# Optimization experiments

Measured on AMD Instinct MI355X. Metric: run time of the kernel, lower is better.

Reference implementation:

```python
import jax, jax.numpy as jnp
import numpy as np

N_NODES = 100000
N_EDGES = 1600000
B = 16
NMAX = 4096
IN_DIM = 32
H1 = 64      # capacity C
H2 = 128     # 2C
LAT = 64
DEC_H = 128  # 2C
DEC_IN = LAT + 2
FUEL = 5


def _ln(x, g, b):
    m = x.mean(-1, keepdims=True)
    v = x.var(-1, keepdims=True)
    return (x - m) / jnp.sqrt(v + 1e-5) * g + b


def _mlp2(x, wi, bi, g, be, wo, bo):
    # DeepMLP with num_layers=2: in_lin -> LayerNorm -> ReLU -> out_lin
    h = jax.nn.relu(_ln(x @ wi + bi, g, be))
    return h @ wo + bo


def setup_inputs() -> dict:
    key = jax.random.key(0)
    ks = jax.random.split(key, 48)
    d = {}
    d['x'] = jax.random.normal(ks[0], (N_NODES, IN_DIM), jnp.float32)
    d['edge_index'] = jax.random.randint(ks[1], (2, N_EDGES), 0, N_NODES)
    d['batch'] = jnp.sort(jax.random.randint(ks[2], (N_NODES,), 0, B))

    def w(k, shape):
        return (jax.random.normal(k, shape, jnp.float32) * 0.02)

    conv_shapes = {'w1m': (IN_DIM, H1), 'w2m': (H1, H2), 'w3m': (H2, LAT),
                   'w1l': (IN_DIM, H1), 'w2l': (H1, H2), 'w3l': (H2, LAT)}
    i = 3
    for nm, sh in conv_shapes.items():
        d[nm] = w(ks[i], sh); i += 1
        d['b' + nm[1:]] = jnp.zeros((sh[1],), jnp.float32)
    # node_mlp (DeepMLP dec_in->dec_h->dec_h)
    d['nm_wi'] = w(ks[i], (DEC_IN, DEC_H)); i += 1
    d['nm_bi'] = jnp.zeros((DEC_H,), jnp.float32)
    d['nm_g'] = jnp.ones((DEC_H,), jnp.float32)
    d['nm_be'] = jnp.zeros((DEC_H,), jnp.float32)
    d['nm_wo'] = w(ks[i], (DEC_H, DEC_H)); i += 1
    d['nm_bo'] = jnp.zeros((DEC_H,), jnp.float32)
    # heads
    d['ex_w'] = w(ks[i], (DEC_H, 1)); i += 1
    d['ex_b'] = jnp.zeros((1,), jnp.float32)
    d['fu_w'] = w(ks[i], (DEC_H, FUEL)); i += 1
    d['fu_b'] = jnp.zeros((FUEL,), jnp.float32)
    d['al_w'] = w(ks[i], (DEC_H, 1)); i += 1
    d['al_b'] = jnp.zeros((1,), jnp.float32)
    d['sl_w'] = w(ks[i], (DEC_H, 1)); i += 1
    d['sl_b'] = jnp.zeros((1,), jnp.float32)
    # edge_mlp (DeepMLP dec_in->dec_h->8)
    d['em_wi'] = w(ks[i], (DEC_IN, DEC_H)); i += 1
    d['em_bi'] = jnp.zeros((DEC_H,), jnp.float32)
    d['em_g'] = jnp.ones((DEC_H,), jnp.float32)
    d['em_be'] = jnp.zeros((DEC_H,), jnp.float32)
    d['em_wo'] = w(ks[i], (DEC_H, 8)); i += 1
    d['em_bo'] = jnp.zeros((8,), jnp.float32)
    d['pos_all'] = jax.random.normal(ks[i], (NMAX, 2), jnp.float32)
    return d


def reference(x, edge_index, batch,
              w1m, b1m, w2m, b2m, w3m, b3m,
              w1l, b1l, w2l, b2l, w3l, b3l,
              nm_wi, nm_bi, nm_g, nm_be, nm_wo, nm_bo,
              ex_w, ex_b, fu_w, fu_b, al_w, al_b, sl_w, sl_b,
              em_wi, em_bi, em_g, em_be, em_wo, em_bo,
              pos_all):
    # ---- GCN encoder with self-loops and symmetric normalization (PyG GCNConv) ----
    loops = jnp.arange(N_NODES)
    src = jnp.concatenate([edge_index[0], loops])
    dst = jnp.concatenate([edge_index[1], loops])
    deg = jax.ops.segment_sum(jnp.ones(src.shape, jnp.float32), dst, N_NODES)
    dinv = jax.lax.rsqrt(deg)  # deg >= 1 because of self-loops
    norm = (dinv[src] * dinv[dst])[:, None]

    def conv(h, wt, bt):
        hw = h @ wt                                   # [N, F_out]
        return jax.ops.segment_sum(norm * hw[src], dst, N_NODES) + bt

    mu = jax.nn.relu(conv(x, w1m, b1m))
    mu = jax.nn.relu(conv(mu, w2m, b2m))
    mu = jax.nn.relu(conv(mu, w3m, b3m))
    lg = jax.nn.relu(conv(x, w1l, b1l))
    lg = jax.nn.relu(conv(lg, w2l, b2l))
    lg = jax.nn.relu(conv(lg, w3l, b3l))

    cnt = jnp.maximum(jax.ops.segment_sum(jnp.ones((N_NODES,), jnp.float32), batch, B), 1.0)[:, None]
    mu_g = jax.ops.segment_sum(mu, batch, B) / cnt    # global_mean_pool [B, LAT]
    lg_g = jax.ops.segment_sum(lg, batch, B) / cnt

    z = mu_g  # eval-mode latent_sample returns mu

    # ---- decoder ----
    Z = jnp.broadcast_to(z[:, None, :], (B, NMAX, LAT))
    pos = jnp.broadcast_to(pos_all[None], (B, NMAX, 2))
    Zp = jnp.concatenate([Z, pos], -1).reshape(B * NMAX, DEC_IN)
    h = _mlp2(Zp, nm_wi, nm_bi, nm_g, nm_be, nm_wo, nm_bo)
    nodes = (h @ ex_w + ex_b).reshape(B, NMAX, 1)
    fuel = (h @ fu_w + fu_b).reshape(B, NMAX, FUEL)
    alt = (h @ al_w + al_b).reshape(B, NMAX, 1)
    slope = (h @ sl_w + sl_b).reshape(B, NMAX, 1)
    edges = _mlp2(Zp, em_wi, em_bi, em_g, em_be, em_wo, em_bo).reshape(B, NMAX, 8)
    return (nodes, edges, fuel, alt, slope, mu_g, lg_g)
```

## Files before the change

### kernel.cpp

```cpp
#include <hip/hip_runtime.h>
#include <hip/hip_bf16.h>

#define N_NODES 100000
#define N_EDGESC 1600000
#define BATCH_B 16
#define NMAXC 4096
#define LATC 64
#define NBINS 391
#define NSB 256
#define EPB ((N_EDGESC + NSB - 1) / NSB)
#define BIN_PAD 768

#define OUT_NODES 0
#define OUT_EDGES 65536
#define OUT_FUEL  589824
#define OUT_ALT   917504
#define OUT_SLOPE 983040
#define OUT_MU    1048576
#define OUT_LG    1049600

typedef float f32x2 __attribute__((ext_vector_type(2)));
typedef float f32x4 __attribute__((ext_vector_type(4)));
typedef short bf16x8 __attribute__((ext_vector_type(8)));
union U4B { uint4 u; bf16x8 b; };

__device__ __forceinline__ unsigned short f2bf(float f) {
    unsigned int u = __float_as_uint(f);
    return (unsigned short)((u + 0x7FFFu + ((u >> 16) & 1u)) >> 16);
}
__device__ __forceinline__ float bf2f(unsigned short h) {
    return __uint_as_float(((unsigned int)h) << 16);
}
__device__ __forceinline__ void f8acc(unsigned int u, float& a0, float& a1, float& a2, float& a3) {
    f32x2 lo = __builtin_amdgcn_cvt_pk_f32_fp8(u, false);
    f32x2 hi = __builtin_amdgcn_cvt_pk_f32_fp8(u, true);
    a0 += lo[0]; a1 += lo[1]; a2 += hi[0]; a3 += hi[1];
}
__device__ __forceinline__ void f8_to_bf2(unsigned int u, unsigned int& q0, unsigned int& q1) {
    f32x2 lo = __builtin_amdgcn_cvt_pk_f32_fp8(u, false);
    f32x2 hi = __builtin_amdgcn_cvt_pk_f32_fp8(u, true);
    q0 = (unsigned int)f2bf(lo[0]) | ((unsigned int)f2bf(lo[1]) << 16);
    q1 = (unsigned int)f2bf(hi[0]) | ((unsigned int)f2bf(hi[1]) << 16);
}

__global__ __launch_bounds__(1024) void histA(const int* __restrict__ dst, int* __restrict__ hist) {
    __shared__ int h[NBINS];
    int b = blockIdx.x, t = threadIdx.x;
    for (int i = t; i < NBINS; i += 1024) h[i] = 0;
    __syncthreads();
    int e0 = b * EPB, e1 = min(e0 + EPB, N_EDGESC);
    for (int i = e0 + t; i < e1; i += 1024)
        atomicAdd(&h[dst[i] >> 8], 1);
    __syncthreads();
    for (int i = t; i < NBINS; i += 1024) hist[i * NSB + b] = h[i];
}

__global__ void scanB(int* __restrict__ hist, int* __restrict__ total) {
    __shared__ int sh[NSB];
    int j = blockIdx.x, t = threadIdx.x;
    int v = hist[j * NSB + t];
    sh[t] = v; __syncthreads();
    for (int off = 1; off < NSB; off <<= 1) {
        int u = (t >= off) ? sh[t - off] : 0; __syncthreads();
        sh[t] += u; __syncthreads();
    }
    hist[j * NSB + t] = sh[t] - v;
    if (t == NSB - 1) total[j] = sh[t];
}

__global__ void scanC(const int* __restrict__ total, int* __restrict__ base) {
    __shared__ int sh[512];
    int t = threadIdx.x;
    int v = (t < NBINS) ? total[t] : 0;
    sh[t] = v; __syncthreads();
    for (int off = 1; off < 512; off <<= 1) {
        int u = (t >= off) ? sh[t - off] : 0; __syncthreads();
        sh[t] += u; __syncthreads();
    }
    if (t < NBINS) base[t] = sh[t] - v;
    if (t == NBINS - 1) base[NBINS] = sh[t];
}

__global__ __launch_bounds__(1024) void scatterD(const int* __restrict__ src, const int* __restrict__ dst,
                                                 const int* __restrict__ hist, const int* __restrict__ base,
                                                 unsigned int* __restrict__ sorted) {
    __shared__ int w0[NBINS];
    __shared__ int lc[NBINS];
    int b = blockIdx.x, t = threadIdx.x;
    for (int i = t; i < NBINS; i += 1024) {
        w0[i] = base[i] + hist[i * NSB + b];
        lc[i] = 0;
    }
    __syncthreads();
    int e0 = b * EPB, e1 = min(e0 + EPB, N_EDGESC);
    for (int i = e0 + t; i < e1; i += 1024) {
        int d = dst[i], s = src[i];
        int j = d >> 8;
        int r = atomicAdd(&lc[j], 1);
        sorted[w0[j] + r] = ((unsigned int)s << 8) | (d & 255);
    }
}

__global__ void csr_compact(const unsigned int* __restrict__ sorted, const int* __restrict__ base,
                            const float* __restrict__ x,
                            int* __restrict__ adj, int2* __restrict__ oc,
                            float* __restrict__ dinv, unsigned int* __restrict__ xs8, int N) {
    __shared__ int lc[256];
    __shared__ int cur[256];
    __shared__ int so4[256];
    int j = blockIdx.x, t = threadIdx.x;
    lc[t] = 0; cur[t] = 0;
    __syncthreads();
    int e0 = base[j], e1 = base[j + 1];
    for (int i = e0 + t; i < e1; i += 256)
        atomicAdd(&lc[sorted[i] & 255], 1);
    __syncthreads();
    int c4 = (lc[t] + 3) & ~3;
    so4[t] = c4;
    __syncthreads();
    for (int off = 1; off < 256; off <<= 1) {
        int u = (t >= off) ? so4[t - off] : 0; __syncthreads();
        so4[t] += u; __syncthreads();
    }
    int mybase = base[j] + j * BIN_PAD + so4[t] - c4;
    __syncthreads();
    so4[t] = mybase;
    __syncthreads();
    for (int i = e0 + t; i < e1; i += 256) {
        unsigned int pk = sorted[i];
        int d = pk & 255;
        int r = atomicAdd(&cur[d], 1);
        adj[so4[d] + r] = (int)(pk >> 8);
    }
    int n = j * 256 + t;
    if (n < N) {
        int c = lc[t];
        oc[n] = make_int2(so4[t], c);
        float dv = rsqrtf((float)(c + 1));
        dinv[n] = dv;
        float ds = dv * 64.f;
        const float* xr = &x[(size_t)n * 32];
        unsigned int q[8];
#pragma unroll
        for (int jj = 0; jj < 8; jj++) {
            float4 v = *(const float4*)&xr[jj * 4];
            unsigned int r8 = 0;
            r8 = __builtin_amdgcn_cvt_pk_fp8_f32(v.x * ds, v.y * ds, r8, false);
            r8 = __builtin_amdgcn_cvt_pk_fp8_f32(v.z * ds, v.w * ds, r8, true);
            q[jj] = r8;
        }
        *(uint4*)&xs8[(size_t)n * 8] = make_uint4(q[0], q[1], q[2], q[3]);
        *(uint4*)&xs8[(size_t)n * 8 + 4] = make_uint4(q[4], q[5], q[6], q[7]);
    }
}

__global__ void agg_s32(const unsigned int* __restrict__ xs8, const int2* __restrict__ oc,
                        const int* __restrict__ adj, const float* __restrict__ dinv,
                        unsigned short* __restrict__ outb, int N) {
    int t = threadIdx.x;
    int sub = t >> 3, f = t & 7;
    int n = blockIdx.x * 32 + sub;
    if (n >= N) return;
    float s0 = 0.f, s1 = 0.f, s2 = 0.f, s3 = 0.f;
    f8acc(xs8[(size_t)n * 8 + f], s0, s1, s2, s3);
    int2 h = oc[n];
    int e = h.x, e1 = h.x + h.y;
    for (; e + 8 <= e1; e += 8) {
        int4 ia = *(const int4*)&adj[e];
        int4 ib = *(const int4*)&adj[e + 4];
        unsigned int u0 = xs8[(size_t)ia.x * 8 + f];
        unsigned int u1 = xs8[(size_t)ia.y * 8 + f];
        unsigned int u2 = xs8[(size_t)ia.z * 8 + f];
        unsigned int u3 = xs8[(size_t)ia.w * 8 + f];
        unsigned int u4 = xs8[(size_t)ib.x * 8 + f];
        unsigned int u5 = xs8[(size_t)ib.y * 8 + f];
        unsigned int u6 = xs8[(size_t)ib.z * 8 + f];
        unsigned int u7 = xs8[(size_t)ib.w * 8 + f];
        f8acc(u0, s0, s1, s2, s3); f8acc(u1, s0, s1, s2, s3);
        f8acc(u2, s0, s1, s2, s3); f8acc(u3, s0, s1, s2, s3);
        f8acc(u4, s0, s1, s2, s3); f8acc(u5, s0, s1, s2, s3);
        f8acc(u6, s0, s1, s2, s3); f8acc(u7, s0, s1, s2, s3);
    }
    if (e + 4 <= e1) {
        int4 ia = *(const int4*)&adj[e];
        unsigned int u0 = xs8[(size_t)ia.x * 8 + f];
        unsigned int u1 = xs8[(size_t)ia.y * 8 + f];
        unsigned int u2 = xs8[(size_t)ia.z * 8 + f];
        unsigned int u3 = xs8[(size_t)ia.w * 8 + f];
        f8acc(u0, s0, s1, s2, s3); f8acc(u1, s0, s1, s2, s3);
        f8acc(u2, s0, s1, s2, s3); f8acc(u3, s0, s1, s2, s3);
        e += 4;
    }
    for (; e < e1; e++) f8acc(xs8[(size_t)adj[e] * 8 + f], s0, s1, s2, s3);
    float d = dinv[n] * (1.f / 64.f);
    ushort4 o;
    o.x = f2bf(s0 * d); o.y = f2bf(s1 * d); o.z = f2bf(s2 * d); o.w = f2bf(s3 * d);
    *(ushort4*)&outb[(size_t)n * 32 + f * 4] = o;
}

template <bool BIASRELU, bool OUT8>
__global__ void agg128(const unsigned int* __restrict__ tbl, const int2* __restrict__ oc,
                       const int* __restrict__ adj, const float* __restrict__ dinv,
                       const float* __restrict__ bias, void* __restrict__ outv, int N) {
    int t = threadIdx.x;
    int sub = t >> 5, f = t & 31;
    int n = blockIdx.x * 8 + sub;
    if (n >= N) return;
    float s0 = 0.f, s1 = 0.f, s2 = 0.f, s3 = 0.f;
    f8acc(tbl[(size_t)n * 32 + f], s0, s1, s2, s3);
    int2 h = oc[n];
    int e = h.x, e1 = h.x + h.y;
    for (; e + 8 <= e1; e += 8) {
        int4 ia = *(const int4*)&adj[e];
        int4 ib = *(const int4*)&adj[e + 4];
        unsigned int u0 = tbl[(size_t)ia.x * 32 + f];
        unsigned int u1 = tbl[(size_t)ia.y * 32 + f];
        unsigned int u2 = tbl[(size_t)ia.z * 32 + f];
        unsigned int u3 = tbl[(size_t)ia.w * 32 + f];
        unsigned int u4 = tbl[(size_t)ib.x * 32 + f];
        unsigned int u5 = tbl[(size_t)ib.y * 32 + f];
        unsigned int u6 = tbl[(size_t)ib.z * 32 + f];
        unsigned int u7 = tbl[(size_t)ib.w * 32 + f];
        f8acc(u0, s0, s1, s2, s3); f8acc(u1, s0, s1, s2, s3);
        f8acc(u2, s0, s1, s2, s3); f8acc(u3, s0, s1, s2, s3);
        f8acc(u4, s0, s1, s2, s3); f8acc(u5, s0, s1, s2, s3);
        f8acc(u6, s0, s1, s2, s3); f8acc(u7, s0, s1, s2, s3);
    }
    if (e + 4 <= e1) {
        int4 ia = *(const int4*)&adj[e];
        unsigned int u0 = tbl[(size_t)ia.x * 32 + f];
        unsigned int u1 = tbl[(size_t)ia.y * 32 + f];
        unsigned int u2 = tbl[(size_t)ia.z * 32 + f];
        unsigned int u3 = tbl[(size_t)ia.w * 32 + f];
        f8acc(u0, s0, s1, s2, s3); f8acc(u1, s0, s1, s2, s3);
        f8acc(u2, s0, s1, s2, s3); f8acc(u3, s0, s1, s2, s3);
        e += 4;
    }
    for (; e < e1; e++) f8acc(tbl[(size_t)adj[e] * 32 + f], s0, s1, s2, s3);
    float d = dinv[n] * (1.f / 32.f);
    float v0 = s0 * d, v1 = s1 * d, v2 = s2 * d, v3 = s3 * d;
    if (BIASRELU) {
        float4 bv = *(const float4*)&bias[4 * f];
        v0 = fmaxf(v0 + bv.x, 0.f); v1 = fmaxf(v1 + bv.y, 0.f);
        v2 = fmaxf(v2 + bv.z, 0.f); v3 = fmaxf(v3 + bv.w, 0.f);
    }
    if (OUT8) {
        unsigned int r = 0;
        r = __builtin_amdgcn_cvt_pk_fp8_f32(v0 * 32.f, v1 * 32.f, r, false);
        r = __builtin_amdgcn_cvt_pk_fp8_f32(v2 * 32.f, v3 * 32.f, r, true);
        ((unsigned int*)outv)[(size_t)n * 32 + f] = r;
    } else {
        ushort4 u;
        u.x = f2bf(v0); u.y = f2bf(v1); u.z = f2bf(v2); u.w = f2bf(v3);
        *(ushort4*)&((unsigned short*)outv)[(size_t)n * 128 + 4 * f] = u;
    }
}

__device__ __forceinline__ void wfrag_write(const float* W, int F, int col, int k0,
                                            unsigned int* dst) {
    unsigned int q[4];
#pragma unroll
    for (int jj = 0; jj < 4; jj++) {
        float lo = W[(size_t)(k0 + 2 * jj) * F + col];
        float hi = W[(size_t)(k0 + 2 * jj + 1) * F + col];
        q[jj] = (unsigned int)f2bf(lo) | ((unsigned int)f2bf(hi) << 16);
    }
    *(uint4*)dst = make_uint4(q[0], q[1], q[2], q[3]);
}

__global__ void mega_prep(const int* __restrict__ batch,
                          const float* __restrict__ w1m, const float* __restrict__ w1l,
                          const float* __restrict__ b1m, const float* __restrict__ b1l,
                          const float* __restrict__ b3m, const float* __restrict__ b3l,
                          const float* __restrict__ w2m, const float* __restrict__ w2l,
                          const float* __restrict__ w3m, const float* __restrict__ w3l,
                          const float* __restrict__ nm_wo, const float* __restrict__ nm_bo,
                          const float* __restrict__ ex_w, const float* __restrict__ ex_b,
                          const float* __restrict__ fu_w, const float* __restrict__ fu_b,
                          const float* __restrict__ al_w, const float* __restrict__ al_b,
                          const float* __restrict__ sl_w, const float* __restrict__ sl_b,
                          const float* __restrict__ em_wo,
                          int* __restrict__ bcnt, float* __restrict__ bcat1,
                          float* __restrict__ bcat3, float* __restrict__ wtn,
                          float* __restrict__ bcn, float* __restrict__ wte,
                          unsigned int* __restrict__ wf1, unsigned int* __restrict__ wf2,
                          unsigned int* __restrict__ wf3) {
    int blk = blockIdx.x, t = threadIdx.x;
    if (blk == 0) {
        if (t < 128) bcat1[t] = (t < 64) ? b1m[t] : b1l[t - 64];
        else { int f = t - 128; bcat3[f] = (f < 64) ? b3m[f] : b3l[f - 64]; }
        if (t < BATCH_B) {
            int b = t;
            int lo = 0, hi = N_NODES;
            while (lo < hi) { int mid = (lo + hi) >> 1; if (batch[mid] < b) lo = mid + 1; else hi = mid; }
            int start = lo;
            lo = 0; hi = N_NODES;
            while (lo < hi) { int mid = (lo + hi) >> 1; if (batch[mid] <= b) lo = mid + 1; else hi = mid; }
            bcnt[b] = lo - start;
        }
    } else if (blk <= 9) {
        int idx = (blk - 1) * 256 + t;
        if (idx < 1024) {
            int j = idx >> 7, k = idx & 127;
            float s = 0.f;
            for (int m = 0; m < 128; m++) {
                float w = (j == 0) ? ex_w[m] : (j <= 5) ? fu_w[m * 5 + (j - 1)]
                         : (j == 6) ? al_w[m] : sl_w[m];
                s += nm_wo[k * 128 + m] * w;
            }
            wtn[j * 128 + k] = s;
        } else if (idx < 2048) {
            int i2 = idx - 1024;
            int j = i2 >> 7, k = i2 & 127;
            wte[j * 128 + k] = em_wo[k * 8 + j];
        } else if (idx < 2056) {
            int j = idx - 2048;
            float s = (j == 0) ? ex_b[0] : (j <= 5) ? fu_b[j - 1] : (j == 6) ? al_b[0] : sl_b[0];
            for (int m = 0; m < 128; m++) {
                float w = (j == 0) ? ex_w[m] : (j <= 5) ? fu_w[m * 5 + (j - 1)]
                         : (j == 6) ? al_w[m] : sl_w[m];
                s += nm_bo[m] * w;
            }
            bcn[j] = s;
        }
    } else if (blk <= 17) {
        if (t < 64) {
            int c = blk - 10;
            int col = c * 16 + (t & 15);
            int k0 = (t >> 4) * 8;
            unsigned int q[4];
#pragma unroll
            for (int jj = 0; jj < 4; jj++) {
                int ka = k0 + 2 * jj, kb = ka + 1;
                float lo = (col < 64) ? w1m[ka * 64 + col] : w1l[ka * 64 + col - 64];
                float hi = (col < 64) ? w1m[kb * 64 + col] : w1l[kb * 64 + col - 64];
                q[jj] = (unsigned int)f2bf(lo) | ((unsigned int)f2bf(hi) << 16);
            }
            *(uint4*)&wf1[((size_t)c * 64 + t) * 4] = make_uint4(q[0], q[1], q[2], q[3]);
        }
    } else if (blk <= 49) {
        if (t < 64) {
            int bc = blk - 18;
            int c = bc % 8, s = (bc / 8) % 2, y = bc / 16;
            const float* W = y ? w2l : w2m;
            wfrag_write(W, 128, c * 16 + (t & 15), s * 32 + (t >> 4) * 8,
                        &wf2[((size_t)bc * 64 + t) * 4]);
        }
    } else {
        if (t < 64) {
            int bc = blk - 50;
            int c = bc % 4, s = (bc / 4) % 4, y = bc / 16;
            const float* W = y ? w3l : w3m;
            wfrag_write(W, 64, c * 16 + (t & 15), s * 32 + (t >> 4) * 8,
                        &wf3[((size_t)bc * 64 + t) * 4]);
        }
    }
}

__global__ __launch_bounds__(256) void mfma_conv1(
    const unsigned short* __restrict__ inv, const unsigned int* __restrict__ wfrag,
    const float* __restrict__ bias, const float* __restrict__ dinv,
    unsigned int* __restrict__ outv, int N) {
    constexpr int C = 8;
    constexpr int FP = 132;
    __shared__ unsigned short buf[4][16][FP];
    int t = threadIdx.x, lane = t & 63, wave = t >> 6;
    int n0 = blockIdx.x * 64 + wave * 16;

    f32x4 acc[C];
#pragma unroll
    for (int c = 0; c < C; c++) acc[c] = (f32x4)(0.f);

    int arow = n0 + (lane & 15);
    bool aok = arow < N;
    U4B af; af.u = make_uint4(0u, 0u, 0u, 0u);
    if (aok)
        af.u = *(const uint4*)(inv + (size_t)arow * 32 + (lane >> 4) * 8);
#pragma unroll
    for (int c = 0; c < C; c++) {
        U4B wb;
        wb.u = *(const uint4*)&wfrag[((size_t)c * 64 + lane) * 4];
        acc[c] = __builtin_amdgcn_mfma_f32_16x16x32_bf16(af.b, wb.b, acc[c], 0, 0, 0);
    }

#pragma unroll
    for (int c = 0; c < C; c++) {
        int col = c * 16 + (lane & 15);
        float bv = bias[col];
#pragma unroll
        for (int r = 0; r < 4; r++) {
            int row = (lane >> 4) * 4 + r;
            int n = n0 + row;
            float v = fmaxf(acc[c][r] + bv, 0.f) * dinv[min(n, N - 1)];
            buf[wave][row][col] = f2bf(v);
        }
    }
    __syncthreads();

    for (int i = t; i < 64 * 16; i += 256) {
        int row = i / 16;
        int f0 = (i % 16) * 8;
        int n = blockIdx.x * 64 + row;
        if (n >= N) continue;
        const unsigned short* bp = &buf[row >> 4][row & 15][f0];
        uint2 a = *(const uint2*)bp;
        uint2 b = *(const uint2*)(bp + 4);
        float e0 = __uint_as_float(a.x << 16), e1 = __uint_as_float(a.x & 0xFFFF0000u);
        float e2 = __uint_as_float(a.y << 16), e3 = __uint_as_float(a.y & 0xFFFF0000u);
        float e4 = __uint_as_float(b.x << 16), e5 = __uint_as_float(b.x & 0xFFFF0000u);
        float e6 = __uint_as_float(b.y << 16), e7 = __uint_as_float(b.y & 0xFFFF0000u);
        unsigned int r0 = 0, r1 = 0;
        r0 = __builtin_amdgcn_cvt_pk_fp8_f32(e0 * 32.f, e1 * 32.f, r0, false);
        r0 = __builtin_amdgcn_cvt_pk_fp8_f32(e2 * 32.f, e3 * 32.f, r0, true);
        r1 = __builtin_amdgcn_cvt_pk_fp8_f32(e4 * 32.f, e5 * 32.f, r1, false);
        r1 = __builtin_amdgcn_cvt_pk_fp8_f32(e6 * 32.f, e7 * 32.f, r1, true);
        *(uint2*)((unsigned char*)outv + (size_t)n * 128 + f0) = make_uint2(r0, r1);
    }
}

__global__ __launch_bounds__(256) void conv23(
    const unsigned int* __restrict__ hB8, const unsigned int* __restrict__ wf2,
    const unsigned int* __restrict__ wf3, const float* __restrict__ b2m,
    const float* __restrict__ b2l, const float* __restrict__ dinv,
    unsigned int* __restrict__ hD8, int N) {
    __shared__ unsigned short hbuf[4][16][136];
    __shared__ unsigned short obuf[4][16][72];
    int t = threadIdx.x, lane = t & 63, wave = t >> 6;
    int y = blockIdx.y;
    int n0 = blockIdx.x * 64 + wave * 16;
    const float* bias = y ? b2l : b2m;
    const unsigned int* w2 = wf2 + (size_t)y * 2 * 8 * 64 * 4;
    const unsigned int* w3 = wf3 + (size_t)y * 4 * 4 * 64 * 4;

    f32x4 acc2[8];
#pragma unroll
    for (int c = 0; c < 8; c++) acc2[c] = (f32x4)(0.f);
    int arow = n0 + (lane & 15);
    bool aok = arow < N;
#pragma unroll
    for (int s = 0; s < 2; s++) {
        U4B af; af.u = make_uint4(0u, 0u, 0u, 0u);
        if (aok) {
            uint2 u = *(const uint2*)((const unsigned char*)hB8 +
                        (size_t)arow * 128 + y * 64 + s * 32 + (lane >> 4) * 8);
            f8_to_bf2(u.x, af.u.x, af.u.y);
            f8_to_bf2(u.y, af.u.z, af.u.w);
        }
#pragma unroll
        for (int c = 0; c < 8; c++) {
            U4B wb;
            wb.u = *(const uint4*)&w2[((size_t)(s * 8 + c) * 64 + lane) * 4];
            acc2[c] = __builtin_amdgcn_mfma_f32_16x16x32_bf16(af.b, wb.b, acc2[c], 0, 0, 0);
        }
    }
#pragma unroll
    for (int c = 0; c < 8; c++) {
        int col = c * 16 + (lane & 15);
        float bv = bias[col];
#pragma unroll
        for (int r = 0; r < 4; r++) {
            int row = (lane >> 4) * 4 + r;
            float v = fmaxf(acc2[c][r] * (1.f / 32.f) + bv, 0.f);
            hbuf[wave][row][col] = f2bf(v);
        }
    }

    f32x4 acc3[4];
#pragma unroll
    for (int c = 0; c < 4; c++) acc3[c] = (f32x4)(0.f);
#pragma unroll
    for (int s = 0; s < 4; s++) {
        U4B af;
        af.u = *(const uint4*)&hbuf[wave][lane & 15][s * 32 + (lane >> 4) * 8];
#pragma unroll
        for (int c = 0; c < 4; c++) {
            U4B wb;
            wb.u = *(const uint4*)&w3[((size_t)(s * 4 + c) * 64 + lane) * 4];
            acc3[c] = __builtin_amdgcn_mfma_f32_16x16x32_bf16(af.b, wb.b, acc3[c], 0, 0, 0);
        }
    }
#pragma unroll
    for (int c = 0; c < 4; c++) {
        int col = c * 16 + (lane & 15);
#pragma unroll
        for (int r = 0; r < 4; r++) {
            int row = (lane >> 4) * 4 + r;
            int n = n0 + row;
            float v = acc3[c][r] * dinv[min(n, N - 1)];
            obuf[wave][row][col] = f2bf(v);
        }
    }
    __syncthreads();
    for (int i = t; i < 64 * 8; i += 256) {
        int row = i / 8;
        int f0 = (i % 8) * 8;
        int n = blockIdx.x * 64 + row;
        if (n >= N) continue;
        const unsigned short* bp = &obuf[row >> 4][row & 15][f0];
        uint2 a = *(const uint2*)bp;
        uint2 b = *(const uint2*)(bp + 4);
        float e0 = __uint_as_float(a.x << 16), e1 = __uint_as_float(a.x & 0xFFFF0000u);
        float e2 = __uint_as_float(a.y << 16), e3 = __uint_as_float(a.y & 0xFFFF0000u);
        float e4 = __uint_as_float(b.x << 16), e5 = __uint_as_float(b.x & 0xFFFF0000u);
        float e6 = __uint_as_float(b.y << 16), e7 = __uint_as_float(b.y & 0xFFFF0000u);
        unsigned int r0 = 0, r1 = 0;
        r0 = __builtin_amdgcn_cvt_pk_fp8_f32(e0 * 32.f, e1 * 32.f, r0, false);
        r0 = __builtin_amdgcn_cvt_pk_fp8_f32(e2 * 32.f, e3 * 32.f, r0, true);
        r1 = __builtin_amdgcn_cvt_pk_fp8_f32(e4 * 32.f, e5 * 32.f, r1, false);
        r1 = __builtin_amdgcn_cvt_pk_fp8_f32(e6 * 32.f, e7 * 32.f, r1, true);
        *(uint2*)((unsigned char*)hD8 + (size_t)n * 128 + y * 64 + f0) = make_uint2(r0, r1);
    }
}

__global__ __launch_bounds__(256) void pool128(const unsigned int* __restrict__ h,
                                               const int* __restrict__ batch,
                                               float* __restrict__ sums, int n) {
    int t = threadIdx.x, lane = t & 63, wave = t >> 6;
    int r0 = blockIdx.x * 64 + wave * 16;
    if (r0 >= n) return;
    int r1 = min(r0 + 16, n);
    int cur = batch[r0];
    float a0 = 0.f, a1 = 0.f;
    for (int i = r0; i < r1; i++) {
        int b = batch[i];
        if (b != cur) {
            atomicAdd(&sums[cur * 128 + 2 * lane], a0);
            atomicAdd(&sums[cur * 128 + 2 * lane + 1], a1);
            a0 = a1 = 0.f; cur = b;
        }
        unsigned int u = h[(size_t)i * 64 + lane];
        a0 += __uint_as_float(u << 16);
        a1 += __uint_as_float(u & 0xFFFF0000u);
    }
    atomicAdd(&sums[cur * 128 + 2 * lane], a0);
    atomicAdd(&sums[cur * 128 + 2 * lane + 1], a1);
}

__global__ void finalize_zwi(const float* __restrict__ sums, const int* __restrict__ bcnt,
                             const float* __restrict__ nm_wi, const float* __restrict__ nm_bi,
                             const float* __restrict__ em_wi, const float* __restrict__ em_bi,
                             float* __restrict__ out, float* __restrict__ zwi_nm,
                             float* __restrict__ zwi_em) {
    __shared__ float zs[64];
    int b = blockIdx.x, t = threadIdx.x;
    float c = fmaxf((float)bcnt[b], 1.f);
    float v = sums[b * 128 + t] / c;
    if (t < 64) { out[OUT_MU + b * 64 + t] = v; zs[t] = v; }
    else out[OUT_LG + b * 64 + (t - 64)] = v;
    __syncthreads();
    float an = nm_bi[t], ae = em_bi[t];
    for (int k = 0; k < 64; k++) {
        float zv = zs[k];
        an += zv * nm_wi[k * 128 + t];
        ae += zv * em_wi[k * 128 + t];
    }
    zwi_nm[b * 128 + t] = an;
    zwi_em[b * 128 + t] = ae;
}

#define D3_ROWS 32

__global__ __launch_bounds__(256) void decoder3(
    const float* __restrict__ zwi_nm, const float* __restrict__ zwi_em,
    const float* __restrict__ nm_wi, const float* __restrict__ em_wi,
    const float* __restrict__ nm_g, const float* __restrict__ nm_be,
    const float* __restrict__ em_g, const float* __restrict__ em_be,
    const float* __restrict__ wtn, const float* __restrict__ bcn,
    const float* __restrict__ wte, const float* __restrict__ em_bo,
    const float* __restrict__ pos_all,
    float* __restrict__ out) {
    __shared__ float sn[D3_ROWS][132];
    __shared__ float se[D3_ROWS][132];
    __shared__ float Wn[8][132];
    __shared__ float We[8][132];
    int t = threadIdx.x;
    int lane = t & 63, wave = t >> 6;
    int rowBase = blockIdx.x * D3_ROWS;
    int b = rowBase >> 12;
    int row0 = rowBase + wave * 8;

    for (int i = t; i < 1024; i += 256) {
        Wn[i >> 7][i & 127] = wtn[i];
        We[i >> 7][i & 127] = wte[i];
    }

    int f0 = lane, f1 = lane + 64;
    float zn0 = zwi_nm[b * 128 + f0], zn1 = zwi_nm[b * 128 + f1];
    float ze0 = zwi_em[b * 128 + f0], ze1 = zwi_em[b * 128 + f1];
    float wn64_0 = nm_wi[64 * 128 + f0], wn64_1 = nm_wi[64 * 128 + f1];
    float wn65_0 = nm_wi[65 * 128 + f0], wn65_1 = nm_wi[65 * 128 + f1];
    float we64_0 = em_wi[64 * 128 + f0], we64_1 = em_wi[64 * 128 + f1];
    float we65_0 = em_wi[65 * 128 + f0], we65_1 = em_wi[65 * 128 + f1];
    float gn0 = nm_g[f0], gn1 = nm_g[f1], bn0 = nm_be[f0], bn1 = nm_be[f1];
    float ge0 = em_g[f0], ge1 = em_g[f1], be0 = em_be[f0], be1 = em_be[f1];

#pragma unroll
    for (int r = 0; r < 8; r++) {
        int row = row0 + r, i = row & (NMAXC - 1);
        float px = pos_all[i * 2], py = pos_all[i * 2 + 1];
        float a0 = zn0 + px * wn64_0 + py * wn65_0;
        float a1 = zn1 + px * wn64_1 + py * wn65_1;
        float e0 = ze0 + px * we64_0 + py * we65_0;
        float e1 = ze1 + px * we64_1 + py * we65_1;
        float sm = a0 + a1, sq = a0 * a0 + a1 * a1;
        float sme = e0 + e1, sqe = e0 * e0 + e1 * e1;
#pragma unroll
        for (int d = 1; d < 64; d <<= 1) {
            sm += __shfl_xor(sm, d); sq += __shfl_xor(sq, d);
            sme += __shfl_xor(sme, d); sqe += __shfl_xor(sqe, d);
        }
        float mean = sm * (1.f / 128.f);
        float var = sq * (1.f / 128.f) - mean * mean;
        float rstd = rsqrtf(var + 1e-5f);
        int rl = wave * 8 + r;
        sn[rl][f0] = fmaxf((a0 - mean) * rstd * gn0 + bn0, 0.f);
        sn[rl][f1] = fmaxf((a1 - mean) * rstd * gn1 + bn1, 0.f);
        float meane = sme * (1.f / 128.f);
        float vare = sqe * (1.f / 128.f) - meane * meane;
        float rstde = rsqrtf(vare + 1e-5f);
        se[rl][f0] = fmaxf((e0 - meane) * rstde * ge0 + be0, 0.f);
        se[rl][f1] = fmaxf((e1 - meane) * rstde * ge1 + be1, 0.f);
    }
    __syncthreads();

    int rl = t >> 3, j = t & 7;
    float accn = 0.f, acce = 0.f;
#pragma unroll 8
    for (int k4 = 0; k4 < 128; k4 += 4) {
        float4 sv = *(const float4*)&sn[rl][k4];
        float4 wv = *(const float4*)&Wn[j][k4];
        float4 sev = *(const float4*)&se[rl][k4];
        float4 wev = *(const float4*)&We[j][k4];
        accn += sv.x * wv.x + sv.y * wv.y + sv.z * wv.z + sv.w * wv.w;
        acce += sev.x * wev.x + sev.y * wev.y + sev.z * wev.z + sev.w * wev.w;
    }
    int row = rowBase + rl;
    accn += bcn[j];
    if (j == 0)       out[OUT_NODES + row] = accn;
    else if (j <= 5)  out[OUT_FUEL + (size_t)row * 5 + (j - 1)] = accn;
    else if (j == 6)  out[OUT_ALT + row] = accn;
    else              out[OUT_SLOPE + row] = accn;
    out[OUT_EDGES + (size_t)row * 8 + j] = acce + em_bo[j];
}

extern "C" void kernel_launch(void* const* d_in, const int* in_sizes, int n_in,
                              void* d_out, int out_size, void* d_ws, size_t ws_size,
                              hipStream_t stream) {
    const float* x    = (const float*)d_in[0];
    const int* edge   = (const int*)d_in[1];
    const int* batch  = (const int*)d_in[2];
    const float* w1m = (const float*)d_in[3];  const float* b1m = (const float*)d_in[4];
    const float* w2m = (const float*)d_in[5];  const float* b2m = (const float*)d_in[6];
    const float* w3m = (const float*)d_in[7];  const float* b3m = (const float*)d_in[8];
    const float* w1l = (const float*)d_in[9];  const float* b1l = (const float*)d_in[10];
    const float* w2l = (const float*)d_in[11]; const float* b2l = (const float*)d_in[12];
    const float* w3l = (const float*)d_in[13]; const float* b3l = (const float*)d_in[14];
    const float* nm_wi = (const float*)d_in[15]; const float* nm_bi = (const float*)d_in[16];
    const float* nm_g  = (const float*)d_in[17]; const float* nm_be = (const float*)d_in[18];
    const float* nm_wo = (const float*)d_in[19]; const float* nm_bo = (const float*)d_in[20];
    const float* ex_w = (const float*)d_in[21]; const float* ex_b = (const float*)d_in[22];
    const float* fu_w = (const float*)d_in[23]; const float* fu_b = (const float*)d_in[24];
    const float* al_w = (const float*)d_in[25]; const float* al_b = (const float*)d_in[26];
    const float* sl_w = (const float*)d_in[27]; const float* sl_b = (const float*)d_in[28];
    const float* em_wi = (const float*)d_in[29]; const float* em_bi = (const float*)d_in[30];
    const float* em_g  = (const float*)d_in[31]; const float* em_be = (const float*)d_in[32];
    const float* em_wo = (const float*)d_in[33]; const float* em_bo = (const float*)d_in[34];
    const float* pos_all = (const float*)d_in[35];
    float* out = (float*)d_out;

    char* p = (char*)d_ws;
    auto alloc = [&](size_t bytes) -> void* {
        void* r = (void*)p;
        p += ((bytes + 255) / 256) * 256;
        return r;
    };
    int2* oc      = (int2*)alloc((size_t)N_NODES * 8);
    float* dinv   = (float*)alloc((size_t)N_NODES * 4);
    int* bcnt     = (int*)alloc(BATCH_B * 4);
    float* sums   = (float*)alloc(BATCH_B * 128 * 4);
    float* zwi_nm = (float*)alloc(BATCH_B * 128 * 4);
    float* zwi_em = (float*)alloc(BATCH_B * 128 * 4);
    float* bcat1  = (float*)alloc(128 * 4);
    float* bcat3  = (float*)alloc(128 * 4);
    float* wtn    = (float*)alloc(8 * 128 * 4);
    float* bcn    = (float*)alloc(8 * 4);
    float* wte    = (float*)alloc(8 * 128 * 4);
    unsigned int* wf1 = (unsigned int*)alloc((size_t)8 * 64 * 4 * 4);
    unsigned int* wf2 = (unsigned int*)alloc((size_t)32 * 64 * 4 * 4);
    unsigned int* wf3 = (unsigned int*)alloc((size_t)32 * 64 * 4 * 4);
    int* hist     = (int*)alloc((size_t)NBINS * NSB * 4);
    int* total    = (int*)alloc((size_t)NBINS * 4);
    int* base     = (int*)alloc((size_t)(NBINS + 1) * 4);
    unsigned int* sorted = (unsigned int*)alloc((size_t)N_EDGESC * 4);
    int* adj      = (int*)alloc((size_t)(N_EDGESC + NBINS * BIN_PAD + 256) * 4);
    unsigned int* xs8 = (unsigned int*)alloc((size_t)N_NODES * 8 * 4);
    unsigned short* agg0b = (unsigned short*)alloc((size_t)N_NODES * 32 * 2);
    unsigned int* hA8 = (unsigned int*)alloc((size_t)N_NODES * 32 * 4);
    unsigned int* hB8 = (unsigned int*)alloc((size_t)N_NODES * 32 * 4);
    unsigned short* final128 = (unsigned short*)alloc((size_t)N_NODES * 128 * 2);
    unsigned int* hD8 = hA8;

    const int* srcp = edge;
    const int* dstp = edge + N_EDGESC;

    hipMemsetAsync(sums, 0, (size_t)BATCH_B * 128 * 4, stream);

    mega_prep<<<82, 256, 0, stream>>>(batch, w1m, w1l, b1m, b1l, b3m, b3l,
                                      w2m, w2l, w3m, w3l, nm_wo, nm_bo,
                                      ex_w, ex_b, fu_w, fu_b, al_w, al_b, sl_w, sl_b,
                                      em_wo, bcnt, bcat1, bcat3, wtn, bcn, wte,
                                      wf1, wf2, wf3);

    histA<<<NSB, 1024, 0, stream>>>(dstp, hist);
    scanB<<<NBINS, NSB, 0, stream>>>(hist, total);
    scanC<<<1, 512, 0, stream>>>(total, base);
    scatterD<<<NSB, 1024, 0, stream>>>(srcp, dstp, hist, base, sorted);
    csr_compact<<<NBINS, 256, 0, stream>>>(sorted, base, x, adj, oc, dinv, xs8, N_NODES);

    agg_s32<<<(N_NODES + 31) / 32, 256, 0, stream>>>(xs8, oc, adj, dinv, agg0b, N_NODES);

    const int GB = (N_NODES + 63) / 64;

    mfma_conv1<<<GB, 256, 0, stream>>>(agg0b, wf1, bcat1, dinv, hA8, N_NODES);

    agg128<false, true><<<(N_NODES + 7) / 8, 256, 0, stream>>>(
        hA8, oc, adj, dinv, nullptr, hB8, N_NODES);

    conv23<<<dim3(GB, 2), 256, 0, stream>>>(hB8, wf2, wf3, b2m, b2l, dinv, hD8, N_NODES);

    agg128<true, false><<<(N_NODES + 7) / 8, 256, 0, stream>>>(
        hD8, oc, adj, dinv, bcat3, final128, N_NODES);

    pool128<<<GB, 256, 0, stream>>>((const unsigned int*)final128, batch, sums, N_NODES);
    finalize_zwi<<<BATCH_B, 128, 0, stream>>>(sums, bcnt, nm_wi, nm_bi, em_wi, em_bi,
                                              out, zwi_nm, zwi_em);

    decoder3<<<BATCH_B * NMAXC / D3_ROWS, 256, 0, stream>>>(
        zwi_nm, zwi_em, nm_wi, em_wi, nm_g, nm_be, em_g, em_be,
        wtn, bcn, wte, em_bo, pos_all, out);
}
```

Measured before the change: 257.2 us.

## Fuse first-layer aggregation into conv1 MFMA and merge prep with histogram

The first-layer neighbour aggregation now runs inside the conv1 MFMA kernel and stages results in shared memory, so the bf16 intermediate buffer and its global round trip go away. The weight-prep kernel and the destination histogram kernel are also merged into one launch with 1024-thread blocks, removing one launch and letting the two independent jobs run together. In exchange, the prep blocks idle most of their 1024 threads, and the fused kernel's shared-memory use may lower occupancy for the latency-bound gather.

Result: no change. 257.1 us (-0.1%).

```diff
diff --git a/kernel.cpp b/kernel.cpp
--- a/kernel.cpp
+++ b/kernel.cpp
@@ -43,16 +43,119 @@
     q1 = (unsigned int)f2bf(hi[0]) | ((unsigned int)f2bf(hi[1]) << 16);
 }
 
-__global__ __launch_bounds__(1024) void histA(const int* __restrict__ dst, int* __restrict__ hist) {
-    __shared__ int h[NBINS];
-    int b = blockIdx.x, t = threadIdx.x;
-    for (int i = t; i < NBINS; i += 1024) h[i] = 0;
-    __syncthreads();
-    int e0 = b * EPB, e1 = min(e0 + EPB, N_EDGESC);
-    for (int i = e0 + t; i < e1; i += 1024)
-        atomicAdd(&h[dst[i] >> 8], 1);
-    __syncthreads();
-    for (int i = t; i < NBINS; i += 1024) hist[i * NSB + b] = h[i];
+__device__ __forceinline__ void wfrag_write(const float* W, int F, int col, int k0,
+                                            unsigned int* dst) {
+    unsigned int q[4];
+#pragma unroll
+    for (int jj = 0; jj < 4; jj++) {
+        float lo = W[(size_t)(k0 + 2 * jj) * F + col];
+        float hi = W[(size_t)(k0 + 2 * jj + 1) * F + col];
+        q[jj] = (unsigned int)f2bf(lo) | ((unsigned int)f2bf(hi) << 16);
+    }
+    *(uint4*)dst = make_uint4(q[0], q[1], q[2], q[3]);
+}
+
+__global__ __launch_bounds__(1024) void prep_hist(
+    const int* __restrict__ batch, const int* __restrict__ dst,
+    const float* __restrict__ w1m, const float* __restrict__ w1l,
+    const float* __restrict__ b1m, const float* __restrict__ b1l,
+    const float* __restrict__ b3m, const float* __restrict__ b3l,
+    const float* __restrict__ w2m, const float* __restrict__ w2l,
+    const float* __restrict__ w3m, const float* __restrict__ w3l,
+    const float* __restrict__ nm_wo, const float* __restrict__ nm_bo,
+    const float* __restrict__ ex_w, const float* __restrict__ ex_b,
+    const float* __restrict__ fu_w, const float* __restrict__ fu_b,
+    const float* __restrict__ al_w, const float* __restrict__ al_b,
+    const float* __restrict__ sl_w, const float* __restrict__ sl_b,
+    const float* __restrict__ em_wo,
+    int* __restrict__ bcnt, float* __restrict__ bcat1,
+    float* __restrict__ bcat3, float* __restrict__ wtn,
+    float* __restrict__ bcn, float* __restrict__ wte,
+    unsigned int* __restrict__ wf1, unsigned int* __restrict__ wf2,
+    unsigned int* __restrict__ wf3, int* __restrict__ hist) {
+    int blk = blockIdx.x, t = threadIdx.x;
+    if (blk >= 82) {
+        __shared__ int h[NBINS];
+        int b = blk - 82;
+        for (int i = t; i < NBINS; i += 1024) h[i] = 0;
+        __syncthreads();
+        int e0 = b * EPB, e1 = min(e0 + EPB, N_EDGESC);
+        for (int i = e0 + t; i < e1; i += 1024)
+            atomicAdd(&h[dst[i] >> 8], 1);
+        __syncthreads();
+        for (int i = t; i < NBINS; i += 1024) hist[i * NSB + b] = h[i];
+        return;
+    }
+    if (t >= 256) return;
+    if (blk == 0) {
+        if (t < 128) bcat1[t] = (t < 64) ? b1m[t] : b1l[t - 64];
+        else { int f = t - 128; bcat3[f] = (f < 64) ? b3m[f] : b3l[f - 64]; }
+        if (t < BATCH_B) {
+            int b = t;
+            int lo = 0, hi = N_NODES;
+            while (lo < hi) { int mid = (lo + hi) >> 1; if (batch[mid] < b) lo = mid + 1; else hi = mid; }
+            int start = lo;
+            lo = 0; hi = N_NODES;
+            while (lo < hi) { int mid = (lo + hi) >> 1; if (batch[mid] <= b) lo = mid + 1; else hi = mid; }
+            bcnt[b] = lo - start;
+        }
+    } else if (blk <= 9) {
+        int idx = (blk - 1) * 256 + t;
+        if (idx < 1024) {
+            int j = idx >> 7, k = idx & 127;
+            float s = 0.f;
+            for (int m = 0; m < 128; m++) {
+                float w = (j == 0) ? ex_w[m] : (j <= 5) ? fu_w[m * 5 + (j - 1)]
+                         : (j == 6) ? al_w[m] : sl_w[m];
+                s += nm_wo[k * 128 + m] * w;
+            }
+            wtn[j * 128 + k] = s;
+        } else if (idx < 2048) {
+            int i2 = idx - 1024;
+            int j = i2 >> 7, k = i2 & 127;
+            wte[j * 128 + k] = em_wo[k * 8 + j];
+        } else if (idx < 2056) {
+            int j = idx - 2048;
+            float s = (j == 0) ? ex_b[0] : (j <= 5) ? fu_b[j - 1] : (j == 6) ? al_b[0] : sl_b[0];
+            for (int m = 0; m < 128; m++) {
+                float w = (j == 0) ? ex_w[m] : (j <= 5) ? fu_w[m * 5 + (j - 1)]
+                         : (j == 6) ? al_w[m] : sl_w[m];
+                s += nm_bo[m] * w;
+            }
+            bcn[j] = s;
+        }
+    } else if (blk <= 17) {
+        if (t < 64) {
+            int c = blk - 10;
+            int col = c * 16 + (t & 15);
+            int k0 = (t >> 4) * 8;
+            unsigned int q[4];
+#pragma unroll
+            for (int jj = 0; jj < 4; jj++) {
+                int ka = k0 + 2 * jj, kb = ka + 1;
+                float lo = (col < 64) ? w1m[ka * 64 + col] : w1l[ka * 64 + col - 64];
+                float hi = (col < 64) ? w1m[kb * 64 + col] : w1l[kb * 64 + col - 64];
+                q[jj] = (unsigned int)f2bf(lo) | ((unsigned int)f2bf(hi) << 16);
+            }
+            *(uint4*)&wf1[((size_t)c * 64 + t) * 4] = make_uint4(q[0], q[1], q[2], q[3]);
+        }
+    } else if (blk <= 49) {
+        if (t < 64) {
+            int bc = blk - 18;
+            int c = bc % 8, s = (bc / 8) % 2, y = bc / 16;
+            const float* W = y ? w2l : w2m;
+            wfrag_write(W, 128, c * 16 + (t & 15), s * 32 + (t >> 4) * 8,
+                        &wf2[((size_t)bc * 64 + t) * 4]);
+        }
+    } else {
+        if (t < 64) {
+            int bc = blk - 50;
+            int c = bc % 4, s = (bc / 4) % 4, y = bc / 16;
+            const float* W = y ? w3l : w3m;
+            wfrag_write(W, 64, c * 16 + (t & 15), s * 32 + (t >> 4) * 8,
+                        &wf3[((size_t)bc * 64 + t) * 4]);
+        }
+    }
 }
 
 __global__ void scanB(int* __restrict__ hist, int* __restrict__ total) {
@@ -154,48 +257,106 @@
     }
 }
 
-__global__ void agg_s32(const unsigned int* __restrict__ xs8, const int2* __restrict__ oc,
-                        const int* __restrict__ adj, const float* __restrict__ dinv,
-                        unsigned short* __restrict__ outb, int N) {
-    int t = threadIdx.x;
-    int sub = t >> 3, f = t & 7;
-    int n = blockIdx.x * 32 + sub;
-    if (n >= N) return;
-    float s0 = 0.f, s1 = 0.f, s2 = 0.f, s3 = 0.f;
-    f8acc(xs8[(size_t)n * 8 + f], s0, s1, s2, s3);
-    int2 h = oc[n];
-    int e = h.x, e1 = h.x + h.y;
-    for (; e + 8 <= e1; e += 8) {
-        int4 ia = *(const int4*)&adj[e];
-        int4 ib = *(const int4*)&adj[e + 4];
-        unsigned int u0 = xs8[(size_t)ia.x * 8 + f];
-        unsigned int u1 = xs8[(size_t)ia.y * 8 + f];
-        unsigned int u2 = xs8[(size_t)ia.z * 8 + f];
-        unsigned int u3 = xs8[(size_t)ia.w * 8 + f];
-        unsigned int u4 = xs8[(size_t)ib.x * 8 + f];
-        unsigned int u5 = xs8[(size_t)ib.y * 8 + f];
-        unsigned int u6 = xs8[(size_t)ib.z * 8 + f];
-        unsigned int u7 = xs8[(size_t)ib.w * 8 + f];
-        f8acc(u0, s0, s1, s2, s3); f8acc(u1, s0, s1, s2, s3);
-        f8acc(u2, s0, s1, s2, s3); f8acc(u3, s0, s1, s2, s3);
-        f8acc(u4, s0, s1, s2, s3); f8acc(u5, s0, s1, s2, s3);
-        f8acc(u6, s0, s1, s2, s3); f8acc(u7, s0, s1, s2, s3);
-    }
-    if (e + 4 <= e1) {
-        int4 ia = *(const int4*)&adj[e];
-        unsigned int u0 = xs8[(size_t)ia.x * 8 + f];
-        unsigned int u1 = xs8[(size_t)ia.y * 8 + f];
-        unsigned int u2 = xs8[(size_t)ia.z * 8 + f];
-        unsigned int u3 = xs8[(size_t)ia.w * 8 + f];
-        f8acc(u0, s0, s1, s2, s3); f8acc(u1, s0, s1, s2, s3);
-        f8acc(u2, s0, s1, s2, s3); f8acc(u3, s0, s1, s2, s3);
-        e += 4;
-    }
-    for (; e < e1; e++) f8acc(xs8[(size_t)adj[e] * 8 + f], s0, s1, s2, s3);
-    float d = dinv[n] * (1.f / 64.f);
-    ushort4 o;
-    o.x = f2bf(s0 * d); o.y = f2bf(s1 * d); o.z = f2bf(s2 * d); o.w = f2bf(s3 * d);
-    *(ushort4*)&outb[(size_t)n * 32 + f * 4] = o;
+__global__ __launch_bounds__(256) void agg_conv1(
+    const unsigned int* __restrict__ xs8, const int2* __restrict__ oc,
+    const int* __restrict__ adj, const float* __restrict__ dinv,
+    const unsigned int* __restrict__ wfrag, const float* __restrict__ bias,
+    unsigned int* __restrict__ outv, int N) {
+    __shared__ unsigned short albuf[64][36];
+    __shared__ unsigned short buf[4][16][132];
+    int t = threadIdx.x, lane = t & 63, wave = t >> 6;
+    int nb0 = blockIdx.x * 64;
+
+#pragma unroll
+    for (int half = 0; half < 2; half++) {
+        int nl = half * 32 + (t >> 3);
+        int f = t & 7;
+        int n = nb0 + nl;
+        ushort4 o = make_ushort4(0, 0, 0, 0);
+        if (n < N) {
+            float s0 = 0.f, s1 = 0.f, s2 = 0.f, s3 = 0.f;
+            f8acc(xs8[(size_t)n * 8 + f], s0, s1, s2, s3);
+            int2 h = oc[n];
+            int e = h.x, e1 = h.x + h.y;
+            for (; e + 8 <= e1; e += 8) {
+                int4 ia = *(const int4*)&adj[e];
+                int4 ib = *(const int4*)&adj[e + 4];
+                unsigned int u0 = xs8[(size_t)ia.x * 8 + f];
+                unsigned int u1 = xs8[(size_t)ia.y * 8 + f];
+                unsigned int u2 = xs8[(size_t)ia.z * 8 + f];
+                unsigned int u3 = xs8[(size_t)ia.w * 8 + f];
+                unsigned int u4 = xs8[(size_t)ib.x * 8 + f];
+                unsigned int u5 = xs8[(size_t)ib.y * 8 + f];
+                unsigned int u6 = xs8[(size_t)ib.z * 8 + f];
+                unsigned int u7 = xs8[(size_t)ib.w * 8 + f];
+                f8acc(u0, s0, s1, s2, s3); f8acc(u1, s0, s1, s2, s3);
+                f8acc(u2, s0, s1, s2, s3); f8acc(u3, s0, s1, s2, s3);
+                f8acc(u4, s0, s1, s2, s3); f8acc(u5, s0, s1, s2, s3);
+                f8acc(u6, s0, s1, s2, s3); f8acc(u7, s0, s1, s2, s3);
+            }
+            if (e + 4 <= e1) {
+                int4 ia = *(const int4*)&adj[e];
+                unsigned int u0 = xs8[(size_t)ia.x * 8 + f];
+                unsigned int u1 = xs8[(size_t)ia.y * 8 + f];
+                unsigned int u2 = xs8[(size_t)ia.z * 8 + f];
+                unsigned int u3 = xs8[(size_t)ia.w * 8 + f];
+                f8acc(u0, s0, s1, s2, s3); f8acc(u1, s0, s1, s2, s3);
+                f8acc(u2, s0, s1, s2, s3); f8acc(u3, s0, s1, s2, s3);
+                e += 4;
+            }
+            for (; e < e1; e++) f8acc(xs8[(size_t)adj[e] * 8 + f], s0, s1, s2, s3);
+            float d = dinv[n] * (1.f / 64.f);
+            o.x = f2bf(s0 * d); o.y = f2bf(s1 * d); o.z = f2bf(s2 * d); o.w = f2bf(s3 * d);
+        }
+        *(ushort4*)&albuf[nl][f * 4] = o;
+    }
+    __syncthreads();
+
+    int n0 = nb0 + wave * 16;
+    f32x4 acc[8];
+#pragma unroll
+    for (int c = 0; c < 8; c++) acc[c] = (f32x4)(0.f);
+    int rl = wave * 16 + (lane & 15);
+    U4B af;
+    af.u = *(const uint4*)&albuf[rl][(lane >> 4) * 8];
+#pragma unroll
+    for (int c = 0; c < 8; c++) {
+        U4B wb;
+        wb.u = *(const uint4*)&wfrag[((size_t)c * 64 + lane) * 4];
+        acc[c] = __builtin_amdgcn_mfma_f32_16x16x32_bf16(af.b, wb.b, acc[c], 0, 0, 0);
+    }
+#pragma unroll
+    for (int c = 0; c < 8; c++) {
+        int col = c * 16 + (lane & 15);
+        float bv = bias[col];
+#pragma unroll
+        for (int r = 0; r < 4; r++) {
+            int row = (lane >> 4) * 4 + r;
+            int n = n0 + row;
+            float v = fmaxf(acc[c][r] + bv, 0.f) * dinv[min(n, N - 1)];
+            buf[wave][row][col] = f2bf(v);
+        }
+    }
+    __syncthreads();
+    for (int i = t; i < 64 * 16; i += 256) {
+        int row = i / 16;
+        int f0 = (i % 16) * 8;
+        int n = nb0 + row;
+        if (n >= N) continue;
+        const unsigned short* bp = &buf[row >> 4][row & 15][f0];
+        uint2 a = *(const uint2*)bp;
+        uint2 b = *(const uint2*)(bp + 4);
+        float e0 = __uint_as_float(a.x << 16), e1 = __uint_as_float(a.x & 0xFFFF0000u);
+        float e2 = __uint_as_float(a.y << 16), e3 = __uint_as_float(a.y & 0xFFFF0000u);
+        float e4 = __uint_as_float(b.x << 16), e5 = __uint_as_float(b.x & 0xFFFF0000u);
+        float e6 = __uint_as_float(b.y << 16), e7 = __uint_as_float(b.y & 0xFFFF0000u);
+        unsigned int r0 = 0, r1 = 0;
+        r0 = __builtin_amdgcn_cvt_pk_fp8_f32(e0 * 32.f, e1 * 32.f, r0, false);
+        r0 = __builtin_amdgcn_cvt_pk_fp8_f32(e2 * 32.f, e3 * 32.f, r0, true);
+        r1 = __builtin_amdgcn_cvt_pk_fp8_f32(e4 * 32.f, e5 * 32.f, r1, false);
+        r1 = __builtin_amdgcn_cvt_pk_fp8_f32(e6 * 32.f, e7 * 32.f, r1, true);
+        *(uint2*)((unsigned char*)outv + (size_t)n * 128 + f0) = make_uint2(r0, r1);
+    }
 }
 
 template <bool BIASRELU, bool OUT8>
@@ -256,168 +417,6 @@
     }
 }
 
-__device__ __forceinline__ void wfrag_write(const float* W, int F, int col, int k0,
-                                            unsigned int* dst) {
-    unsigned int q[4];
-#pragma unroll
-    for (int jj = 0; jj < 4; jj++) {
-        float lo = W[(size_t)(k0 + 2 * jj) * F + col];
-        float hi = W[(size_t)(k0 + 2 * jj + 1) * F + col];
-        q[jj] = (unsigned int)f2bf(lo) | ((unsigned int)f2bf(hi) << 16);
-    }
-    *(uint4*)dst = make_uint4(q[0], q[1], q[2], q[3]);
-}
-
-__global__ void mega_prep(const int* __restrict__ batch,
-                          const float* __restrict__ w1m, const float* __restrict__ w1l,
-                          const float* __restrict__ b1m, const float* __restrict__ b1l,
-                          const float* __restrict__ b3m, const float* __restrict__ b3l,
-                          const float* __restrict__ w2m, const float* __restrict__ w2l,
-                          const float* __restrict__ w3m, const float* __restrict__ w3l,
-                          const float* __restrict__ nm_wo, const float* __restrict__ nm_bo,
-                          const float* __restrict__ ex_w, const float* __restrict__ ex_b,
-                          const float* __restrict__ fu_w, const float* __restrict__ fu_b,
-                          const float* __restrict__ al_w, const float* __restrict__ al_b,
-                          const float* __restrict__ sl_w, const float* __restrict__ sl_b,
-                          const float* __restrict__ em_wo,
-                          int* __restrict__ bcnt, float* __restrict__ bcat1,
-                          float* __restrict__ bcat3, float* __restrict__ wtn,
-                          float* __restrict__ bcn, float* __restrict__ wte,
-                          unsigned int* __restrict__ wf1, unsigned int* __restrict__ wf2,
-                          unsigned int* __restrict__ wf3) {
-    int blk = blockIdx.x, t = threadIdx.x;
-    if (blk == 0) {
-        if (t < 128) bcat1[t] = (t < 64) ? b1m[t] : b1l[t - 64];
-        else { int f = t - 128; bcat3[f] = (f < 64) ? b3m[f] : b3l[f - 64]; }
-        if (t < BATCH_B) {
-            int b = t;
-            int lo = 0, hi = N_NODES;
-            while (lo < hi) { int mid = (lo + hi) >> 1; if (batch[mid] < b) lo = mid + 1; else hi = mid; }
-            int start = lo;
-            lo = 0; hi = N_NODES;
-            while (lo < hi) { int mid = (lo + hi) >> 1; if (batch[mid] <= b) lo = mid + 1; else hi = mid; }
-            bcnt[b] = lo - start;
-        }
-    } else if (blk <= 9) {
-        int idx = (blk - 1) * 256 + t;
-        if (idx < 1024) {
-            int j = idx >> 7, k = idx & 127;
-            float s = 0.f;
-            for (int m = 0; m < 128; m++) {
-                float w = (j == 0) ? ex_w[m] : (j <= 5) ? fu_w[m * 5 + (j - 1)]
-                         : (j == 6) ? al_w[m] : sl_w[m];
-                s += nm_wo[k * 128 + m] * w;
-            }
-            wtn[j * 128 + k] = s;
-        } else if (idx < 2048) {
-            int i2 = idx - 1024;
-            int j = i2 >> 7, k = i2 & 127;
-            wte[j * 128 + k] = em_wo[k * 8 + j];
-        } else if (idx < 2056) {
-            int j = idx - 2048;
-            float s = (j == 0) ? ex_b[0] : (j <= 5) ? fu_b[j - 1] : (j == 6) ? al_b[0] : sl_b[0];
-            for (int m = 0; m < 128; m++) {
-                float w = (j == 0) ? ex_w[m] : (j <= 5) ? fu_w[m * 5 + (j - 1)]
-                         : (j == 6) ? al_w[m] : sl_w[m];
-                s += nm_bo[m] * w;
-            }
-            bcn[j] = s;
-        }
-    } else if (blk <= 17) {
-        if (t < 64) {
-            int c = blk - 10;
-            int col = c * 16 + (t & 15);
-            int k0 = (t >> 4) * 8;
-            unsigned int q[4];
-#pragma unroll
-            for (int jj = 0; jj < 4; jj++) {
-                int ka = k0 + 2 * jj, kb = ka + 1;
-                float lo = (col < 64) ? w1m[ka * 64 + col] : w1l[ka * 64 + col - 64];
-                float hi = (col < 64) ? w1m[kb * 64 + col] : w1l[kb * 64 + col - 64];
-                q[jj] = (unsigned int)f2bf(lo) | ((unsigned int)f2bf(hi) << 16);
-            }
-            *(uint4*)&wf1[((size_t)c * 64 + t) * 4] = make_uint4(q[0], q[1], q[2], q[3]);
-        }
-    } else if (blk <= 49) {
-        if (t < 64) {
-            int bc = blk - 18;
-            int c = bc % 8, s = (bc / 8) % 2, y = bc / 16;
-            const float* W = y ? w2l : w2m;
-            wfrag_write(W, 128, c * 16 + (t & 15), s * 32 + (t >> 4) * 8,
-                        &wf2[((size_t)bc * 64 + t) * 4]);
-        }
-    } else {
-        if (t < 64) {
-            int bc = blk - 50;
-            int c = bc % 4, s = (bc / 4) % 4, y = bc / 16;
-            const float* W = y ? w3l : w3m;
-            wfrag_write(W, 64, c * 16 + (t & 15), s * 32 + (t >> 4) * 8,
-                        &wf3[((size_t)bc * 64 + t) * 4]);
-        }
-    }
-}
-
-__global__ __launch_bounds__(256) void mfma_conv1(
-    const unsigned short* __restrict__ inv, const unsigned int* __restrict__ wfrag,
-    const float* __restrict__ bias, const float* __restrict__ dinv,
-    unsigned int* __restrict__ outv, int N) {
-    constexpr int C = 8;
-    constexpr int FP = 132;
-    __shared__ unsigned short buf[4][16][FP];
-    int t = threadIdx.x, lane = t & 63, wave = t >> 6;
-    int n0 = blockIdx.x * 64 + wave * 16;
-
-    f32x4 acc[C];
-#pragma unroll
-    for (int c = 0; c < C; c++) acc[c] = (f32x4)(0.f);
-
-    int arow = n0 + (lane & 15);
-    bool aok = arow < N;
-    U4B af; af.u = make_uint4(0u, 0u, 0u, 0u);
-    if (aok)
-        af.u = *(const uint4*)(inv + (size_t)arow * 32 + (lane >> 4) * 8);
-#pragma unroll
-    for (int c = 0; c < C; c++) {
-        U4B wb;
-        wb.u = *(const uint4*)&wfrag[((size_t)c * 64 + lane) * 4];
-        acc[c] = __builtin_amdgcn_mfma_f32_16x16x32_bf16(af.b, wb.b, acc[c], 0, 0, 0);
-    }
-
-#pragma unroll
-    for (int c = 0; c < C; c++) {
-        int col = c * 16 + (lane & 15);
-        float bv = bias[col];
-#pragma unroll
-        for (int r = 0; r < 4; r++) {
-            int row = (lane >> 4) * 4 + r;
-            int n = n0 + row;
-            float v = fmaxf(acc[c][r] + bv, 0.f) * dinv[min(n, N - 1)];
-            buf[wave][row][col] = f2bf(v);
-        }
-    }
-    __syncthreads();
-
-    for (int i = t; i < 64 * 16; i += 256) {
-        int row = i / 16;
-        int f0 = (i % 16) * 8;
-        int n = blockIdx.x * 64 + row;
-        if (n >= N) continue;
-        const unsigned short* bp = &buf[row >> 4][row & 15][f0];
-        uint2 a = *(const uint2*)bp;
-        uint2 b = *(const uint2*)(bp + 4);
-        float e0 = __uint_as_float(a.x << 16), e1 = __uint_as_float(a.x & 0xFFFF0000u);
-        float e2 = __uint_as_float(a.y << 16), e3 = __uint_as_float(a.y & 0xFFFF0000u);
-        float e4 = __uint_as_float(b.x << 16), e5 = __uint_as_float(b.x & 0xFFFF0000u);
-        float e6 = __uint_as_float(b.y << 16), e7 = __uint_as_float(b.y & 0xFFFF0000u);
-        unsigned int r0 = 0, r1 = 0;
-        r0 = __builtin_amdgcn_cvt_pk_fp8_f32(e0 * 32.f, e1 * 32.f, r0, false);
-        r0 = __builtin_amdgcn_cvt_pk_fp8_f32(e2 * 32.f, e3 * 32.f, r0, true);
-        r1 = __builtin_amdgcn_cvt_pk_fp8_f32(e4 * 32.f, e5 * 32.f, r1, false);
-        r1 = __builtin_amdgcn_cvt_pk_fp8_f32(e6 * 32.f, e7 * 32.f, r1, true);
-        *(uint2*)((unsigned char*)outv + (size_t)n * 128 + f0) = make_uint2(r0, r1);
-    }
-}
-
 __global__ __launch_bounds__(256) void conv23(
     const unsigned int* __restrict__ hB8, const unsigned int* __restrict__ wf2,
     const unsigned int* __restrict__ wf3, const float* __restrict__ b2m,
@@ -694,7 +693,6 @@
     unsigned int* sorted = (unsigned int*)alloc((size_t)N_EDGESC * 4);
     int* adj      = (int*)alloc((size_t)(N_EDGESC + NBINS * BIN_PAD + 256) * 4);
     unsigned int* xs8 = (unsigned int*)alloc((size_t)N_NODES * 8 * 4);
-    unsigned short* agg0b = (unsigned short*)alloc((size_t)N_NODES * 32 * 2);
     unsigned int* hA8 = (unsigned int*)alloc((size_t)N_NODES * 32 * 4);
     unsigned int* hB8 = (unsigned int*)alloc((size_t)N_NODES * 32 * 4);
     unsigned short* final128 = (unsigned short*)alloc((size_t)N_NODES * 128 * 2);
@@ -705,23 +703,20 @@
 
     hipMemsetAsync(sums, 0, (size_t)BATCH_B * 128 * 4, stream);
 
-    mega_prep<<<82, 256, 0, stream>>>(batch, w1m, w1l, b1m, b1l, b3m, b3l,
-                                      w2m, w2l, w3m, w3l, nm_wo, nm_bo,
-                                      ex_w, ex_b, fu_w, fu_b, al_w, al_b, sl_w, sl_b,
-                                      em_wo, bcnt, bcat1, bcat3, wtn, bcn, wte,
-                                      wf1, wf2, wf3);
-
-    histA<<<NSB, 1024, 0, stream>>>(dstp, hist);
+    prep_hist<<<82 + NSB, 1024, 0, stream>>>(batch, dstp, w1m, w1l, b1m, b1l, b3m, b3l,
+                                             w2m, w2l, w3m, w3l, nm_wo, nm_bo,
+                                             ex_w, ex_b, fu_w, fu_b, al_w, al_b, sl_w, sl_b,
+                                             em_wo, bcnt, bcat1, bcat3, wtn, bcn, wte,
+                                             wf1, wf2, wf3, hist);
+
     scanB<<<NBINS, NSB, 0, stream>>>(hist, total);
     scanC<<<1, 512, 0, stream>>>(total, base);
     scatterD<<<NSB, 1024, 0, stream>>>(srcp, dstp, hist, base, sorted);
     csr_compact<<<NBINS, 256, 0, stream>>>(sorted, base, x, adj, oc, dinv, xs8, N_NODES);
 
-    agg_s32<<<(N_NODES + 31) / 32, 256, 0, stream>>>(xs8, oc, adj, dinv, agg0b, N_NODES);
-
     const int GB = (N_NODES + 63) / 64;
 
-    mfma_conv1<<<GB, 256, 0, stream>>>(agg0b, wf1, bcat1, dinv, hA8, N_NODES);
+    agg_conv1<<<GB, 256, 0, stream>>>(xs8, oc, adj, dinv, wf1, bcat1, hA8, N_NODES);
 
     agg128<false, true><<<(N_NODES + 7) / 8, 256, 0, stream>>>(
         hA8, oc, adj, dinv, nullptr, hB8, N_NODES);
```
